# Optimization experiments

Measured on AMD Instinct MI355X. Metric: run time of the kernel, lower is better.

The kernel has to match this reference:

```python
import jax, jax.numpy as jnp
import numpy as np

N, E, G = 50000, 800000, 128
IN_DIM, HID, HEADS, OUT_DIM = 256, 64, 4, 10
HC = HID * HEADS  # 256
NEG_SLOPE = 0.2


def _gat_layer(x, src, dst, W, att_src, att_dst, bias):
    # x: [N, F_in]; W: [F_in, H*C]; att_*: [H, C]; bias: [H*C]
    n = x.shape[0]
    h = (x @ W).reshape(n, HEADS, HID)                      # [N,H,C]
    a_src = jnp.einsum('nhc,hc->nh', h, att_src)            # [N,H]
    a_dst = jnp.einsum('nhc,hc->nh', h, att_dst)            # [N,H]
    e = a_src[src] + a_dst[dst]                             # [E,H]
    e = jax.nn.leaky_relu(e, NEG_SLOPE)
    # segment softmax over incoming edges of each dst node
    m = jax.ops.segment_max(e, dst, num_segments=n)         # [N,H]
    ex = jnp.exp(e - m[dst])
    denom = jax.ops.segment_sum(ex, dst, num_segments=n)    # [N,H]
    alpha = ex / (denom[dst] + 1e-16)                       # [E,H]
    msg = h[src] * alpha[:, :, None]                        # [E,H,C]
    out = jax.ops.segment_sum(msg, dst, num_segments=n)     # [N,H,C]
    return out.reshape(n, HC) + bias


def setup_inputs() -> dict:
    key = jax.random.key(0)
    ks = jax.random.split(key, 16)
    x = jax.random.normal(ks[0], (N, IN_DIM), dtype=jnp.float32)
    edge_index = jax.random.randint(ks[1], (2, E), 0, N, dtype=jnp.int64)
    edge_weight = jax.random.uniform(ks[2], (E,), dtype=jnp.float32)
    batch = jnp.sort(jax.random.randint(ks[3], (N,), 0, G, dtype=jnp.int64))
    s = 0.05
    W1 = jax.random.normal(ks[4], (IN_DIM, HC), dtype=jnp.float32) * s
    att_src1 = jax.random.normal(ks[5], (HEADS, HID), dtype=jnp.float32) * s
    att_dst1 = jax.random.normal(ks[6], (HEADS, HID), dtype=jnp.float32) * s
    b1 = jnp.zeros((HC,), dtype=jnp.float32)
    W2 = jax.random.normal(ks[7], (HC, HC), dtype=jnp.float32) * s
    att_src2 = jax.random.normal(ks[8], (HEADS, HID), dtype=jnp.float32) * s
    att_dst2 = jax.random.normal(ks[9], (HEADS, HID), dtype=jnp.float32) * s
    b2 = jnp.zeros((HC,), dtype=jnp.float32)
    Wf = jax.random.normal(ks[10], (HC, OUT_DIM), dtype=jnp.float32) * s
    bf = jnp.zeros((OUT_DIM,), dtype=jnp.float32)
    return dict(x=x, edge_index=edge_index, edge_weight=edge_weight, batch=batch,
                W1=W1, att_src1=att_src1, att_dst1=att_dst1, b1=b1,
                W2=W2, att_src2=att_src2, att_dst2=att_dst2, b2=b2,
                Wf=Wf, bf=bf)


def reference(x, edge_index, edge_weight, batch,
              W1, att_src1, att_dst1, b1,
              W2, att_src2, att_dst2, b2,
              Wf, bf):
    n = x.shape[0]
    # add self loops (add_self_loops=True in GATConv)
    loop = jnp.arange(n, dtype=edge_index.dtype)
    ei = jnp.concatenate([edge_index, jnp.stack([loop, loop])], axis=1)
    src, dst = ei[0], ei[1]
    h = jax.nn.relu(_gat_layer(x, src, dst, W1, att_src1, att_dst1, b1))
    h = jax.nn.relu(_gat_layer(h, src, dst, W2, att_src2, att_dst2, b2))
    # global mean pool per graph
    counts = jax.ops.segment_sum(jnp.ones((n,), dtype=h.dtype), batch, num_segments=G)
    pooled = jax.ops.segment_sum(h, batch, num_segments=G) / jnp.maximum(counts, 1.0)[:, None]
    out = pooled @ Wf + bf
    return out, pooled
```

## Files before the change

### kernel.cpp

```cpp
#include <hip/hip_runtime.h>
#include <math.h>

#define HEADS 4
#define HID 64
#define HC 256
#define NEG_SLOPE 0.2f
#define GG 128

typedef __attribute__((ext_vector_type(8))) short short8;
typedef __attribute__((ext_vector_type(4))) float floatx4;

__device__ __forceinline__ unsigned short f2bf(float f) {
  unsigned u = __float_as_uint(f);
  unsigned r = (u + 0x7FFFu + ((u >> 16) & 1u)) >> 16;
  return (unsigned short)r;
}
__device__ __forceinline__ float bf2f(unsigned short h) {
  return __uint_as_float(((unsigned)h) << 16);
}

__global__ void fill_counts_kernel(int* counts, int n) {
  int i = blockIdx.x * 256 + threadIdx.x;
  if (i < n) counts[i] = 1;
}

__global__ void hist_kernel(const int* __restrict__ ei, int* counts, int E) {
  int e = blockIdx.x * 256 + threadIdx.x;
  if (e < E) atomicAdd(&counts[ei[E + e]], 1);
}

__global__ __launch_bounds__(256) void scan_pass1(const int* __restrict__ counts,
                                                  int* __restrict__ bsums, int n) {
  int t = threadIdx.x;
  int i0 = blockIdx.x * 1024 + t * 4;
  int s = 0;
  if (i0 + 3 < n) {
    int4 v = *(const int4*)&counts[i0];
    s = v.x + v.y + v.z + v.w;
  } else {
#pragma unroll
    for (int k = 0; k < 4; ++k)
      if (i0 + k < n) s += counts[i0 + k];
  }
#pragma unroll
  for (int o = 1; o < 64; o <<= 1) s += __shfl_xor(s, o, 64);
  __shared__ int ws[4];
  if ((t & 63) == 0) ws[t >> 6] = s;
  __syncthreads();
  if (t == 0) bsums[blockIdx.x] = ws[0] + ws[1] + ws[2] + ws[3];
}

__global__ __launch_bounds__(256) void scan_pass2(int* __restrict__ bsums,
                                                  int* __restrict__ row_ptr, int nb, int n) {
  __shared__ int sh[256];
  int t = threadIdx.x;
  int v = (t < nb) ? bsums[t] : 0;
  sh[t] = v;
  __syncthreads();
  for (int off = 1; off < 256; off <<= 1) {
    int u = (t >= off) ? sh[t - off] : 0;
    __syncthreads();
    sh[t] += u;
    __syncthreads();
  }
  if (t < nb) bsums[t] = sh[t] - v;
  if (t == 255) row_ptr[n] = sh[255];
}

__global__ __launch_bounds__(256) void scan_pass3(const int* __restrict__ counts,
                                                  const int* __restrict__ bsums,
                                                  int* __restrict__ row_ptr,
                                                  int* __restrict__ cursor, int n) {
  int t = threadIdx.x;
  int i0 = blockIdx.x * 1024 + t * 4;
  int c0 = 0, c1 = 0, c2 = 0, c3 = 0;
  bool full = (i0 + 3 < n);
  if (full) {
    int4 v = *(const int4*)&counts[i0];
    c0 = v.x; c1 = v.y; c2 = v.z; c3 = v.w;
  } else {
    if (i0 + 0 < n) c0 = counts[i0 + 0];
    if (i0 + 1 < n) c1 = counts[i0 + 1];
    if (i0 + 2 < n) c2 = counts[i0 + 2];
    if (i0 + 3 < n) c3 = counts[i0 + 3];
  }
  int ts = c0 + c1 + c2 + c3;
  __shared__ int sh[256];
  sh[t] = ts;
  __syncthreads();
  for (int off = 1; off < 256; off <<= 1) {
    int u = (t >= off) ? sh[t - off] : 0;
    __syncthreads();
    sh[t] += u;
    __syncthreads();
  }
  int run = bsums[blockIdx.x] + sh[t] - ts;
  int r0 = run, r1 = run + c0, r2 = r1 + c1, r3 = r2 + c2;
  if (full) {
    *(int4*)&row_ptr[i0] = make_int4(r0, r1, r2, r3);
    *(int4*)&cursor[i0] = make_int4(r0, r1, r2, r3);
  } else {
    if (i0 + 0 < n) { row_ptr[i0 + 0] = r0; cursor[i0 + 0] = r0; }
    if (i0 + 1 < n) { row_ptr[i0 + 1] = r1; cursor[i0 + 1] = r1; }
    if (i0 + 2 < n) { row_ptr[i0 + 2] = r2; cursor[i0 + 2] = r2; }
    if (i0 + 3 < n) { row_ptr[i0 + 3] = r3; cursor[i0 + 3] = r3; }
  }
}

__global__ void scatter_kernel(const int* __restrict__ ei, int* cursor, int* srcs, int E, int n) {
  int i = blockIdx.x * 256 + threadIdx.x;
  if (i >= E + n) return;
  int s, d;
  if (i < E) { s = ei[i]; d = ei[E + i]; }
  else       { s = i - E; d = s; }
  int pos = atomicAdd(&cursor[d], 1);
  srcs[pos] = s;
}

__global__ void convertB_kernel(const float* __restrict__ B, unsigned short* __restrict__ Bth,
                                unsigned short* __restrict__ Btl) {
  int k = blockIdx.x, n = threadIdx.x;
  float v = B[k * HC + n];
  unsigned short h = f2bf(v);
  unsigned short l = f2bf(v - bf2f(h));
  Bth[n * HC + k] = h;
  Btl[n * HC + k] = l;
}

#define LDA 40
__global__ __launch_bounds__(256) void gemm_kernel(
    const float* __restrict__ A, const unsigned short* __restrict__ Bth,
    const unsigned short* __restrict__ Btl, const float* __restrict__ att_src,
    const float* __restrict__ att_dst, unsigned short* __restrict__ Cb,
    float* __restrict__ asrc_o, float* __restrict__ adst_o, int M) {
  __shared__ unsigned short sAh[128 * LDA];
  __shared__ unsigned short sAl[128 * LDA];
  __shared__ unsigned short sBh[128 * LDA];
  __shared__ unsigned short sBl[128 * LDA];

  int t = threadIdx.x;
  int lane = t & 63, wave = t >> 6;
  int wm = wave >> 1, wn = wave & 1;
  int q = lane >> 4, mrow = lane & 15;
  int r0 = blockIdx.y * 128;
  int c0 = blockIdx.x * 128;

  int arow = t >> 1;
  int aofs = (t & 1) * 16;
  bool avalid = (r0 + arow) < M;
  const float* Ag = A + (size_t)(r0 + arow) * HC + aofs;
  const unsigned short* Bgh = Bth + (size_t)(c0 + arow) * HC + aofs;
  const unsigned short* Bgl = Btl + (size_t)(c0 + arow) * HC + aofs;

  floatx4 acc[4][4];
#pragma unroll
  for (int i = 0; i < 4; ++i)
#pragma unroll
    for (int j = 0; j < 4; ++j) acc[i][j] = (floatx4)(0.0f);

  for (int k0 = 0; k0 < HC; k0 += 32) {
    __syncthreads();
#pragma unroll
    for (int c = 0; c < 16; c += 4) {
      float4 v = make_float4(0.f, 0.f, 0.f, 0.f);
      if (avalid) v = *(const float4*)(Ag + k0 + c);
      unsigned short h0 = f2bf(v.x), h1 = f2bf(v.y), h2 = f2bf(v.z), h3 = f2bf(v.w);
      ushort4 hv = make_ushort4(h0, h1, h2, h3);
      ushort4 lv = make_ushort4(f2bf(v.x - bf2f(h0)), f2bf(v.y - bf2f(h1)),
                                f2bf(v.z - bf2f(h2)), f2bf(v.w - bf2f(h3)));
      *(ushort4*)&sAh[arow * LDA + aofs + c] = hv;
      *(ushort4*)&sAl[arow * LDA + aofs + c] = lv;
    }
    *(int4*)&sBh[arow * LDA + aofs] = *(const int4*)(Bgh + k0);
    *(int4*)&sBh[arow * LDA + aofs + 8] = *(const int4*)(Bgh + k0 + 8);
    *(int4*)&sBl[arow * LDA + aofs] = *(const int4*)(Bgl + k0);
    *(int4*)&sBl[arow * LDA + aofs + 8] = *(const int4*)(Bgl + k0 + 8);
    __syncthreads();

    short8 ah[4], al[4], bh[4], bl[4];
#pragma unroll
    for (int i = 0; i < 4; ++i) {
      int ar = (wm * 64 + i * 16 + mrow) * LDA + q * 8;
      int br = (wn * 64 + i * 16 + mrow) * LDA + q * 8;
      ah[i] = *(short8*)&sAh[ar];
      al[i] = *(short8*)&sAl[ar];
      bh[i] = *(short8*)&sBh[br];
      bl[i] = *(short8*)&sBl[br];
    }
#pragma unroll
    for (int i = 0; i < 4; ++i)
#pragma unroll
      for (int j = 0; j < 4; ++j) {
        acc[i][j] = __builtin_amdgcn_mfma_f32_16x16x32_bf16(ah[i], bh[j], acc[i][j], 0, 0, 0);
        acc[i][j] = __builtin_amdgcn_mfma_f32_16x16x32_bf16(ah[i], bl[j], acc[i][j], 0, 0, 0);
        acc[i][j] = __builtin_amdgcn_mfma_f32_16x16x32_bf16(al[i], bh[j], acc[i][j], 0, 0, 0);
      }
  }

  int hd = (c0 >> 6) + wn;
  float aS[4], aD[4];
#pragma unroll
  for (int j = 0; j < 4; ++j) {
    aS[j] = att_src[hd * 64 + j * 16 + mrow];
    aD[j] = att_dst[hd * 64 + j * 16 + mrow];
  }
#pragma unroll
  for (int i = 0; i < 4; ++i) {
#pragma unroll
    for (int r = 0; r < 4; ++r) {
      float ps = acc[i][0][r] * aS[0] + acc[i][1][r] * aS[1] +
                 acc[i][2][r] * aS[2] + acc[i][3][r] * aS[3];
      float pd = acc[i][0][r] * aD[0] + acc[i][1][r] * aD[1] +
                 acc[i][2][r] * aD[2] + acc[i][3][r] * aD[3];
#pragma unroll
      for (int o = 1; o < 16; o <<= 1) {
        ps += __shfl_xor(ps, o, 64);
        pd += __shfl_xor(pd, o, 64);
      }
      int grow = r0 + wm * 64 + i * 16 + q * 4 + r;
      if (mrow == 0 && grow < M) {
        asrc_o[grow * HEADS + hd] = ps;
        adst_o[grow * HEADS + hd] = pd;
      }
    }
  }

#pragma unroll
  for (int i = 0; i < 4; ++i) {
#pragma unroll
    for (int j = 0; j < 4; ++j) {
      int col = c0 + wn * 64 + j * 16 + mrow;
#pragma unroll
      for (int r = 0; r < 4; ++r) {
        int grow = r0 + wm * 64 + i * 16 + q * 4 + r;
        if (grow < M) Cb[(size_t)grow * HC + col] = f2bf(acc[i][j][r]);
      }
    }
  }
}

__device__ __forceinline__ float lrelu(float x) { return x > 0.f ? x : NEG_SLOPE * x; }

__global__ __launch_bounds__(256) void aggregate_kernel(
    const unsigned short* __restrict__ hbf, const float* __restrict__ asrc,
    const float* __restrict__ adst, const int* __restrict__ row_ptr,
    const int* __restrict__ srcs, const float* __restrict__ bias,
    float* __restrict__ hout, int N) {
  __shared__ float s_alpha[4][64 * 4];
  __shared__ int s_src[4][64];

  int wave = threadIdx.x >> 6;
  int lane = threadIdx.x & 63;
  int node = blockIdx.x * 4 + wave;
  if (node >= N) return;

  int begin = row_ptr[node];
  int end = row_ptr[node + 1];
  int deg = end - begin;
  int nb = deg < 64 ? deg : 64;

  const float4* asrc4 = (const float4*)asrc;
  float4 ad = ((const float4*)adst)[node];

  const float NEGINF = -3.402823466e38f;
  int s0 = 0;
  float4 e0 = make_float4(NEGINF, NEGINF, NEGINF, NEGINF);
  if (lane < nb) {
    s0 = srcs[begin + lane];
    float4 a = asrc4[s0];
    e0.x = lrelu(a.x + ad.x);
    e0.y = lrelu(a.y + ad.y);
    e0.z = lrelu(a.z + ad.z);
    e0.w = lrelu(a.w + ad.w);
  }
  float m0 = e0.x, m1 = e0.y, m2 = e0.z, m3 = e0.w;
  for (int base = 64; base < deg; base += 64) {
    int idx = base + lane;
    if (idx < deg) {
      int s = srcs[begin + idx];
      float4 a = asrc4[s];
      m0 = fmaxf(m0, lrelu(a.x + ad.x));
      m1 = fmaxf(m1, lrelu(a.y + ad.y));
      m2 = fmaxf(m2, lrelu(a.z + ad.z));
      m3 = fmaxf(m3, lrelu(a.w + ad.w));
    }
  }
#pragma unroll
  for (int o = 1; o < 64; o <<= 1) {
    m0 = fmaxf(m0, __shfl_xor(m0, o, 64));
    m1 = fmaxf(m1, __shfl_xor(m1, o, 64));
    m2 = fmaxf(m2, __shfl_xor(m2, o, 64));
    m3 = fmaxf(m3, __shfl_xor(m3, o, 64));
  }
  float ex0 = (lane < nb) ? __expf(e0.x - m0) : 0.f;
  float ex1 = (lane < nb) ? __expf(e0.y - m1) : 0.f;
  float ex2 = (lane < nb) ? __expf(e0.z - m2) : 0.f;
  float ex3 = (lane < nb) ? __expf(e0.w - m3) : 0.f;
  float d0 = ex0, d1 = ex1, d2 = ex2, d3 = ex3;
  for (int base = 64; base < deg; base += 64) {
    int idx = base + lane;
    if (idx < deg) {
      int s = srcs[begin + idx];
      float4 a = asrc4[s];
      d0 += __expf(lrelu(a.x + ad.x) - m0);
      d1 += __expf(lrelu(a.y + ad.y) - m1);
      d2 += __expf(lrelu(a.z + ad.z) - m2);
      d3 += __expf(lrelu(a.w + ad.w) - m3);
    }
  }
#pragma unroll
  for (int o = 1; o < 64; o <<= 1) {
    d0 += __shfl_xor(d0, o, 64);
    d1 += __shfl_xor(d1, o, 64);
    d2 += __shfl_xor(d2, o, 64);
    d3 += __shfl_xor(d3, o, 64);
  }
  float r0 = 1.0f / (d0 + 1e-16f);
  float r1 = 1.0f / (d1 + 1e-16f);
  float r2 = 1.0f / (d2 + 1e-16f);
  float r3 = 1.0f / (d3 + 1e-16f);

  *(float4*)&s_alpha[wave][lane * 4] = make_float4(ex0 * r0, ex1 * r1, ex2 * r2, ex3 * r3);
  s_src[wave][lane] = s0;

  int head = lane >> 4;
  float mh = (head == 0) ? m0 : (head == 1) ? m1 : (head == 2) ? m2 : m3;
  float rdh = (head == 0) ? r0 : (head == 1) ? r1 : (head == 2) ? r2 : r3;
  float adh = (head == 0) ? ad.x : (head == 1) ? ad.y : (head == 2) ? ad.z : ad.w;

  const ushort4* hb4 = (const ushort4*)hbf;
  float4 accA = make_float4(0.f, 0.f, 0.f, 0.f);
  float4 accB = accA, accC = accA, accD = accA;
  int i = 0;
  for (; i + 4 <= nb; i += 4) {
    int sa = s_src[wave][i];
    int sb = s_src[wave][i + 1];
    int sc = s_src[wave][i + 2];
    int sd = s_src[wave][i + 3];
    float aa = s_alpha[wave][i * 4 + head];
    float ab = s_alpha[wave][(i + 1) * 4 + head];
    float ac = s_alpha[wave][(i + 2) * 4 + head];
    float ad_ = s_alpha[wave][(i + 3) * 4 + head];
    ushort4 u0 = hb4[(size_t)sa * 64 + lane];
    ushort4 u1 = hb4[(size_t)sb * 64 + lane];
    ushort4 u2 = hb4[(size_t)sc * 64 + lane];
    ushort4 u3 = hb4[(size_t)sd * 64 + lane];
    accA.x += aa * bf2f(u0.x); accA.y += aa * bf2f(u0.y);
    accA.z += aa * bf2f(u0.z); accA.w += aa * bf2f(u0.w);
    accB.x += ab * bf2f(u1.x); accB.y += ab * bf2f(u1.y);
    accB.z += ab * bf2f(u1.z); accB.w += ab * bf2f(u1.w);
    accC.x += ac * bf2f(u2.x); accC.y += ac * bf2f(u2.y);
    accC.z += ac * bf2f(u2.z); accC.w += ac * bf2f(u2.w);
    accD.x += ad_ * bf2f(u3.x); accD.y += ad_ * bf2f(u3.y);
    accD.z += ad_ * bf2f(u3.z); accD.w += ad_ * bf2f(u3.w);
  }
  for (; i < nb; ++i) {
    int s = s_src[wave][i];
    float a = s_alpha[wave][i * 4 + head];
    ushort4 u = hb4[(size_t)s * 64 + lane];
    accA.x += a * bf2f(u.x); accA.y += a * bf2f(u.y);
    accA.z += a * bf2f(u.z); accA.w += a * bf2f(u.w);
  }
  for (int i2 = 64; i2 < deg; ++i2) {
    int s = srcs[begin + i2];
    float ash = asrc[s * HEADS + head];
    float a = __expf(lrelu(ash + adh) - mh) * rdh;
    ushort4 u = hb4[(size_t)s * 64 + lane];
    accA.x += a * bf2f(u.x); accA.y += a * bf2f(u.y);
    accA.z += a * bf2f(u.z); accA.w += a * bf2f(u.w);
  }

  float4 acc;
  acc.x = (accA.x + accB.x) + (accC.x + accD.x);
  acc.y = (accA.y + accB.y) + (accC.y + accD.y);
  acc.z = (accA.z + accB.z) + (accC.z + accD.z);
  acc.w = (accA.w + accB.w) + (accC.w + accD.w);
  float4 bv = ((const float4*)bias)[lane];
  float4 o;
  o.x = fmaxf(acc.x + bv.x, 0.f);
  o.y = fmaxf(acc.y + bv.y, 0.f);
  o.z = fmaxf(acc.z + bv.z, 0.f);
  o.w = fmaxf(acc.w + bv.w, 0.f);
  ((float4*)hout)[(size_t)node * 64 + lane] = o;
}

__device__ __forceinline__ int lower_bound_i(const int* a, int n, int key) {
  int lo = 0, hi = n;
  while (lo < hi) {
    int mid = (lo + hi) >> 1;
    if (a[mid] < key) lo = mid + 1; else hi = mid;
  }
  return lo;
}

__global__ __launch_bounds__(256) void pool_kernel(const float* __restrict__ h2,
                                                   const int* __restrict__ batch,
                                                   float* __restrict__ pooled, int n) {
  int g = blockIdx.x;
  int wave = threadIdx.x >> 6, lane = threadIdx.x & 63;
  int lo = lower_bound_i(batch, n, g);
  int hi = lower_bound_i(batch, n, g + 1);
  const float4* h4 = (const float4*)h2;
  float4 acc = make_float4(0.f, 0.f, 0.f, 0.f);
  for (int i = lo + wave; i < hi; i += 4) {
    float4 v = h4[(size_t)i * 64 + lane];
    acc.x += v.x; acc.y += v.y; acc.z += v.z; acc.w += v.w;
  }
  __shared__ float4 red[4][64];
  red[wave][lane] = acc;
  __syncthreads();
  if (wave == 0) {
    float4 a0 = red[0][lane], a1 = red[1][lane], a2 = red[2][lane], a3 = red[3][lane];
    float inv = 1.0f / fmaxf((float)(hi - lo), 1.0f);
    float4 o;
    o.x = (a0.x + a1.x + a2.x + a3.x) * inv;
    o.y = (a0.y + a1.y + a2.y + a3.y) * inv;
    o.z = (a0.z + a1.z + a2.z + a3.z) * inv;
    o.w = (a0.w + a1.w + a2.w + a3.w) * inv;
    ((float4*)pooled)[g * 64 + lane] = o;
  }
}

__global__ void final_kernel(const float* __restrict__ pooled, const float* __restrict__ Wf,
                             const float* __restrict__ bf, float* __restrict__ out) {
  int g = blockIdx.x, t = threadIdx.x;
  __shared__ float p[HC];
  p[t] = pooled[g * HC + t];
  __syncthreads();
  if (t < 10) {
    float s = bf[t];
    for (int c = 0; c < HC; ++c) s += p[c] * Wf[c * 10 + t];
    out[g * 10 + t] = s;
  }
}

extern "C" void kernel_launch(void* const* d_in, const int* in_sizes, int n_in,
                              void* d_out, int out_size, void* d_ws, size_t ws_size,
                              hipStream_t stream) {
  const float* x    = (const float*)d_in[0];
  const int*   ei   = (const int*)d_in[1];
  const int*   batch = (const int*)d_in[3];
  const float* W1   = (const float*)d_in[4];
  const float* as1  = (const float*)d_in[5];
  const float* ad1  = (const float*)d_in[6];
  const float* b1   = (const float*)d_in[7];
  const float* W2   = (const float*)d_in[8];
  const float* as2  = (const float*)d_in[9];
  const float* ad2  = (const float*)d_in[10];
  const float* b2   = (const float*)d_in[11];
  const float* Wf   = (const float*)d_in[12];
  const float* bf   = (const float*)d_in[13];
  float* out = (float*)d_out;

  const int N = in_sizes[0] / HC;
  const int E = in_sizes[1] / 2;

  float* bufB = (float*)d_ws;
  unsigned short* hbf = (unsigned short*)(bufB + (size_t)N * HC);
  float* asrc = (float*)(hbf + (size_t)N * HC);
  float* adst = asrc + (size_t)N * HEADS;
  int* counts = (int*)(adst + (size_t)N * HEADS);
  int* row_ptr = counts + N;
  int* cursor = row_ptr + N + 1;
  int* srcs = cursor + N;
  int* bsums = srcs + E + N;
  unsigned short* Bth = (unsigned short*)(bsums + ((N + 1023) / 1024 + 4));
  unsigned short* Btl = Bth + HC * HC;

  int nb = (N + 1023) / 1024;

  fill_counts_kernel<<<(N + 255) / 256, 256, 0, stream>>>(counts, N);
  hist_kernel<<<(E + 255) / 256, 256, 0, stream>>>(ei, counts, E);
  scan_pass1<<<nb, 256, 0, stream>>>(counts, bsums, N);
  scan_pass2<<<1, 256, 0, stream>>>(bsums, row_ptr, nb, N);
  scan_pass3<<<nb, 256, 0, stream>>>(counts, bsums, row_ptr, cursor, N);
  scatter_kernel<<<(E + N + 255) / 256, 256, 0, stream>>>(ei, cursor, srcs, E, N);

  dim3 ggrid(2, (N + 127) / 128);
  int agg_blocks = (N + 3) / 4;

  convertB_kernel<<<HC, HC, 0, stream>>>(W1, Bth, Btl);
  gemm_kernel<<<ggrid, 256, 0, stream>>>(x, Bth, Btl, as1, ad1, hbf, asrc, adst, N);
  aggregate_kernel<<<agg_blocks, 256, 0, stream>>>(hbf, asrc, adst, row_ptr, srcs, b1, bufB, N);

  convertB_kernel<<<HC, HC, 0, stream>>>(W2, Bth, Btl);
  gemm_kernel<<<ggrid, 256, 0, stream>>>(bufB, Bth, Btl, as2, ad2, hbf, asrc, adst, N);
  aggregate_kernel<<<agg_blocks, 256, 0, stream>>>(hbf, asrc, adst, row_ptr, srcs, b2, bufB, N);

  pool_kernel<<<GG, 256, 0, stream>>>(bufB, batch, out + GG * 10, N);
  final_kernel<<<GG, 256, 0, stream>>>(out + GG * 10, Wf, bf, out);
}
```

Measured before the change: 495.4 us.

## Pre-split GEMM A operand into bf16 hi/lo and parallelize pooling

Adds a splitA kernel that converts x into bf16 high/low halves once, and has layer-1 aggregation write its output directly as bf16 hi/lo. The GEMM then loads pre-split bf16 tiles with int4 loads instead of converting fp32 inside the inner loop. Pooling is split across 4 partial blocks per graph, and the final kernel reduces the partials. The intent is to remove redundant per-tile conversion (A was re-split for each of the 2 column blocks) and raise pooling parallelism. The cost is an extra pass over x and a reworked workspace layout.

```diff
diff --git a/kernel.cpp b/kernel.cpp
--- a/kernel.cpp
+++ b/kernel.cpp
@@ -9,13 +9,14 @@
 
 typedef __attribute__((ext_vector_type(8))) short short8;
 typedef __attribute__((ext_vector_type(4))) float floatx4;
-
-__device__ __forceinline__ unsigned short f2bf(float f) {
+typedef unsigned short ush;
+
+__device__ __forceinline__ ush f2bf(float f) {
   unsigned u = __float_as_uint(f);
   unsigned r = (u + 0x7FFFu + ((u >> 16) & 1u)) >> 16;
-  return (unsigned short)r;
-}
-__device__ __forceinline__ float bf2f(unsigned short h) {
+  return (ush)r;
+}
+__device__ __forceinline__ float bf2f(ush h) {
   return __uint_as_float(((unsigned)h) << 16);
 }
 
@@ -117,26 +118,47 @@
   srcs[pos] = s;
 }
 
-__global__ void convertB_kernel(const float* __restrict__ B, unsigned short* __restrict__ Bth,
-                                unsigned short* __restrict__ Btl) {
+__global__ __launch_bounds__(256) void splitA_kernel(const float* __restrict__ A,
+                                                     ush* __restrict__ Ah,
+                                                     ush* __restrict__ Al, int total) {
+  int i0 = (blockIdx.x * 256 + threadIdx.x) * 4;
+  if (i0 + 3 < total) {
+    float4 v = *(const float4*)&A[i0];
+    ushort4 h = make_ushort4(f2bf(v.x), f2bf(v.y), f2bf(v.z), f2bf(v.w));
+    ushort4 l = make_ushort4(f2bf(v.x - bf2f(h.x)), f2bf(v.y - bf2f(h.y)),
+                             f2bf(v.z - bf2f(h.z)), f2bf(v.w - bf2f(h.w)));
+    *(ushort4*)&Ah[i0] = h;
+    *(ushort4*)&Al[i0] = l;
+  } else {
+    for (int k = 0; k < 4 && i0 + k < total; ++k) {
+      float v = A[i0 + k];
+      ush h = f2bf(v);
+      Ah[i0 + k] = h;
+      Al[i0 + k] = f2bf(v - bf2f(h));
+    }
+  }
+}
+
+__global__ void convertB_kernel(const float* __restrict__ B, ush* __restrict__ Bth,
+                                ush* __restrict__ Btl) {
   int k = blockIdx.x, n = threadIdx.x;
   float v = B[k * HC + n];
-  unsigned short h = f2bf(v);
-  unsigned short l = f2bf(v - bf2f(h));
+  ush h = f2bf(v);
+  ush l = f2bf(v - bf2f(h));
   Bth[n * HC + k] = h;
   Btl[n * HC + k] = l;
 }
 
 #define LDA 40
 __global__ __launch_bounds__(256) void gemm_kernel(
-    const float* __restrict__ A, const unsigned short* __restrict__ Bth,
-    const unsigned short* __restrict__ Btl, const float* __restrict__ att_src,
-    const float* __restrict__ att_dst, unsigned short* __restrict__ Cb,
-    float* __restrict__ asrc_o, float* __restrict__ adst_o, int M) {
-  __shared__ unsigned short sAh[128 * LDA];
-  __shared__ unsigned short sAl[128 * LDA];
-  __shared__ unsigned short sBh[128 * LDA];
-  __shared__ unsigned short sBl[128 * LDA];
+    const ush* __restrict__ Ah, const ush* __restrict__ Al,
+    const ush* __restrict__ Bth, const ush* __restrict__ Btl,
+    const float* __restrict__ att_src, const float* __restrict__ att_dst,
+    ush* __restrict__ Cb, float* __restrict__ asrc_o, float* __restrict__ adst_o, int M) {
+  __shared__ ush sAh[128 * LDA];
+  __shared__ ush sAl[128 * LDA];
+  __shared__ ush sBh[128 * LDA];
+  __shared__ ush sBl[128 * LDA];
 
   int t = threadIdx.x;
   int lane = t & 63, wave = t >> 6;
@@ -145,12 +167,10 @@
   int r0 = blockIdx.y * 128;
   int c0 = blockIdx.x * 128;
 
-  int arow = t >> 1;
-  int aofs = (t & 1) * 16;
-  bool avalid = (r0 + arow) < M;
-  const float* Ag = A + (size_t)(r0 + arow) * HC + aofs;
-  const unsigned short* Bgh = Bth + (size_t)(c0 + arow) * HC + aofs;
-  const unsigned short* Bgl = Btl + (size_t)(c0 + arow) * HC + aofs;
+  int row0 = t >> 2, seg0 = t & 3;
+  int row1 = (t + 256) >> 2, seg1 = (t + 256) & 3;
+  bool v0 = (r0 + row0) < M, v1 = (r0 + row1) < M;
+  const int4 zero4 = make_int4(0, 0, 0, 0);
 
   floatx4 acc[4][4];
 #pragma unroll
@@ -160,21 +180,20 @@
 
   for (int k0 = 0; k0 < HC; k0 += 32) {
     __syncthreads();
-#pragma unroll
-    for (int c = 0; c < 16; c += 4) {
-      float4 v = make_float4(0.f, 0.f, 0.f, 0.f);
-      if (avalid) v = *(const float4*)(Ag + k0 + c);
-      unsigned short h0 = f2bf(v.x), h1 = f2bf(v.y), h2 = f2bf(v.z), h3 = f2bf(v.w);
-      ushort4 hv = make_ushort4(h0, h1, h2, h3);
-      ushort4 lv = make_ushort4(f2bf(v.x - bf2f(h0)), f2bf(v.y - bf2f(h1)),
-                                f2bf(v.z - bf2f(h2)), f2bf(v.w - bf2f(h3)));
-      *(ushort4*)&sAh[arow * LDA + aofs + c] = hv;
-      *(ushort4*)&sAl[arow * LDA + aofs + c] = lv;
-    }
-    *(int4*)&sBh[arow * LDA + aofs] = *(const int4*)(Bgh + k0);
-    *(int4*)&sBh[arow * LDA + aofs + 8] = *(const int4*)(Bgh + k0 + 8);
-    *(int4*)&sBl[arow * LDA + aofs] = *(const int4*)(Bgl + k0);
-    *(int4*)&sBl[arow * LDA + aofs + 8] = *(const int4*)(Bgl + k0 + 8);
+    {
+      size_t g0 = (size_t)(r0 + row0) * HC + k0 + seg0 * 8;
+      size_t g1 = (size_t)(r0 + row1) * HC + k0 + seg1 * 8;
+      *(int4*)&sAh[row0 * LDA + seg0 * 8] = v0 ? *(const int4*)&Ah[g0] : zero4;
+      *(int4*)&sAh[row1 * LDA + seg1 * 8] = v1 ? *(const int4*)&Ah[g1] : zero4;
+      *(int4*)&sAl[row0 * LDA + seg0 * 8] = v0 ? *(const int4*)&Al[g0] : zero4;
+      *(int4*)&sAl[row1 * LDA + seg1 * 8] = v1 ? *(const int4*)&Al[g1] : zero4;
+      size_t b0 = (size_t)(c0 + row0) * HC + k0 + seg0 * 8;
+      size_t b1 = (size_t)(c0 + row1) * HC + k0 + seg1 * 8;
+      *(int4*)&sBh[row0 * LDA + seg0 * 8] = *(const int4*)&Bth[b0];
+      *(int4*)&sBh[row1 * LDA + seg1 * 8] = *(const int4*)&Bth[b1];
+      *(int4*)&sBl[row0 * LDA + seg0 * 8] = *(const int4*)&Btl[b0];
+      *(int4*)&sBl[row1 * LDA + seg1 * 8] = *(const int4*)&Btl[b1];
+    }
     __syncthreads();
 
     short8 ah[4], al[4], bh[4], bl[4];
@@ -242,10 +261,10 @@
 __device__ __forceinline__ float lrelu(float x) { return x > 0.f ? x : NEG_SLOPE * x; }
 
 __global__ __launch_bounds__(256) void aggregate_kernel(
-    const unsigned short* __restrict__ hbf, const float* __restrict__ asrc,
+    const ush* __restrict__ hbf, const float* __restrict__ asrc,
     const float* __restrict__ adst, const int* __restrict__ row_ptr,
     const int* __restrict__ srcs, const float* __restrict__ bias,
-    float* __restrict__ hout, int N) {
+    float* __restrict__ outf, ush* __restrict__ outh, ush* __restrict__ outl, int N) {
   __shared__ float s_alpha[4][64 * 4];
   __shared__ int s_src[4][64];
 
@@ -381,7 +400,16 @@
   o.y = fmaxf(acc.y + bv.y, 0.f);
   o.z = fmaxf(acc.z + bv.z, 0.f);
   o.w = fmaxf(acc.w + bv.w, 0.f);
-  ((float4*)hout)[(size_t)node * 64 + lane] = o;
+
+  if (outf) {
+    ((float4*)outf)[(size_t)node * 64 + lane] = o;
+  } else {
+    ushort4 h = make_ushort4(f2bf(o.x), f2bf(o.y), f2bf(o.z), f2bf(o.w));
+    ushort4 l = make_ushort4(f2bf(o.x - bf2f(h.x)), f2bf(o.y - bf2f(h.y)),
+                             f2bf(o.z - bf2f(h.z)), f2bf(o.w - bf2f(h.w)));
+    ((ushort4*)outh)[(size_t)node * 64 + lane] = h;
+    ((ushort4*)outl)[(size_t)node * 64 + lane] = l;
+  }
 }
 
 __device__ __forceinline__ int lower_bound_i(const int* a, int n, int key) {
@@ -395,14 +423,15 @@
 
 __global__ __launch_bounds__(256) void pool_kernel(const float* __restrict__ h2,
                                                    const int* __restrict__ batch,
-                                                   float* __restrict__ pooled, int n) {
-  int g = blockIdx.x;
+                                                   float* __restrict__ pws,
+                                                   int* __restrict__ cnts, int n) {
+  int g = blockIdx.x, part = blockIdx.y;
   int wave = threadIdx.x >> 6, lane = threadIdx.x & 63;
   int lo = lower_bound_i(batch, n, g);
   int hi = lower_bound_i(batch, n, g + 1);
   const float4* h4 = (const float4*)h2;
   float4 acc = make_float4(0.f, 0.f, 0.f, 0.f);
-  for (int i = lo + wave; i < hi; i += 4) {
+  for (int i = lo + part * 4 + wave; i < hi; i += 16) {
     float4 v = h4[(size_t)i * 64 + lane];
     acc.x += v.x; acc.y += v.y; acc.z += v.z; acc.w += v.w;
   }
@@ -411,26 +440,32 @@
   __syncthreads();
   if (wave == 0) {
     float4 a0 = red[0][lane], a1 = red[1][lane], a2 = red[2][lane], a3 = red[3][lane];
-    float inv = 1.0f / fmaxf((float)(hi - lo), 1.0f);
     float4 o;
-    o.x = (a0.x + a1.x + a2.x + a3.x) * inv;
-    o.y = (a0.y + a1.y + a2.y + a3.y) * inv;
-    o.z = (a0.z + a1.z + a2.z + a3.z) * inv;
-    o.w = (a0.w + a1.w + a2.w + a3.w) * inv;
-    ((float4*)pooled)[g * 64 + lane] = o;
-  }
-}
-
-__global__ void final_kernel(const float* __restrict__ pooled, const float* __restrict__ Wf,
-                             const float* __restrict__ bf, float* __restrict__ out) {
+    o.x = (a0.x + a1.x) + (a2.x + a3.x);
+    o.y = (a0.y + a1.y) + (a2.y + a3.y);
+    o.z = (a0.z + a1.z) + (a2.z + a3.z);
+    o.w = (a0.w + a1.w) + (a2.w + a3.w);
+    ((float4*)pws)[(size_t)(g * 4 + part) * 64 + lane] = o;
+  }
+  if (part == 0 && threadIdx.x == 0) cnts[g] = hi - lo;
+}
+
+__global__ void final_kernel(const float* __restrict__ pws, const int* __restrict__ cnts,
+                             const float* __restrict__ Wf, const float* __restrict__ bf,
+                             float* __restrict__ pooled_out, float* __restrict__ out) {
   int g = blockIdx.x, t = threadIdx.x;
+  float s = pws[(size_t)(g * 4 + 0) * 256 + t] + pws[(size_t)(g * 4 + 1) * 256 + t] +
+            pws[(size_t)(g * 4 + 2) * 256 + t] + pws[(size_t)(g * 4 + 3) * 256 + t];
+  float inv = 1.0f / fmaxf((float)cnts[g], 1.0f);
+  float pv = s * inv;
+  pooled_out[g * HC + t] = pv;
   __shared__ float p[HC];
-  p[t] = pooled[g * HC + t];
+  p[t] = pv;
   __syncthreads();
   if (t < 10) {
-    float s = bf[t];
-    for (int c = 0; c < HC; ++c) s += p[c] * Wf[c * 10 + t];
-    out[g * 10 + t] = s;
+    float acc = bf[t];
+    for (int c = 0; c < HC; ++c) acc += p[c] * Wf[c * 10 + t];
+    out[g * 10 + t] = acc;
   }
 }
 
@@ -455,17 +490,28 @@
   const int N = in_sizes[0] / HC;
   const int E = in_sizes[1] / 2;
 
-  float* bufB = (float*)d_ws;
-  unsigned short* hbf = (unsigned short*)(bufB + (size_t)N * HC);
-  float* asrc = (float*)(hbf + (size_t)N * HC);
-  float* adst = asrc + (size_t)N * HEADS;
-  int* counts = (int*)(adst + (size_t)N * HEADS);
-  int* row_ptr = counts + N;
-  int* cursor = row_ptr + N + 1;
-  int* srcs = cursor + N;
-  int* bsums = srcs + E + N;
-  unsigned short* Bth = (unsigned short*)(bsums + ((N + 1023) / 1024 + 4));
-  unsigned short* Btl = Bth + HC * HC;
+  char* base = (char*)d_ws;
+  size_t off = 0;
+  auto alloc = [&](size_t bytes) {
+    char* p = base + off;
+    off = (off + bytes + 255) & ~(size_t)255;
+    return p;
+  };
+  ush* xh = (ush*)alloc((size_t)N * HC * 2);
+  ush* xl = (ush*)alloc((size_t)N * HC * 2);
+  float* bufB = (float*)xh;
+  ush* hbf = (ush*)alloc((size_t)N * HC * 2);
+  float* asrc = (float*)alloc((size_t)N * HEADS * 4);
+  float* adst = (float*)alloc((size_t)N * HEADS * 4);
+  int* counts = (int*)alloc((size_t)N * 4);
+  int* row_ptr = (int*)alloc((size_t)(N + 1) * 4);
+  int* cursor = (int*)alloc((size_t)N * 4);
+  int* srcs = (int*)alloc((size_t)(E + N) * 4);
+  int* bsums = (int*)alloc(((N + 1023) / 1024) * 4);
+  ush* Bth = (ush*)alloc((size_t)HC * HC * 2);
+  ush* Btl = (ush*)alloc((size_t)HC * HC * 2);
+  float* pws = (float*)alloc((size_t)GG * 4 * HC * 4);
+  int* cnts = (int*)alloc((size_t)GG * 4);
 
   int nb = (N + 1023) / 1024;
 
@@ -479,14 +525,19 @@
   dim3 ggrid(2, (N + 127) / 128);
   int agg_blocks = (N + 3) / 4;
 
+  splitA_kernel<<<(N * HC / 4 + 255) / 256, 256, 0, stream>>>(x, xh, xl, N * HC);
+
   convertB_kernel<<<HC, HC, 0, stream>>>(W1, Bth, Btl);
-  gemm_kernel<<<ggrid, 256, 0, stream>>>(x, Bth, Btl, as1, ad1, hbf, asrc, adst, N);
-  aggregate_kernel<<<agg_blocks, 256, 0, stream>>>(hbf, asrc, adst, row_ptr, srcs, b1, bufB, N);
+  gemm_kernel<<<ggrid, 256, 0, stream>>>(xh, xl, Bth, Btl, as1, ad1, hbf, asrc, adst, N);
+  aggregate_kernel<<<agg_blocks, 256, 0, stream>>>(hbf, asrc, adst, row_ptr, srcs, b1,
+                                                   nullptr, xh, xl, N);
 
   convertB_kernel<<<HC, HC, 0, stream>>>(W2, Bth, Btl);
-  gemm_kernel<<<ggrid, 256, 0, stream>>>(bufB, Bth, Btl, as2, ad2, hbf, asrc, adst, N);
-  aggregate_kernel<<<agg_blocks, 256, 0, stream>>>(hbf, asrc, adst, row_ptr, srcs, b2, bufB, N);
-
-  pool_kernel<<<GG, 256, 0, stream>>>(bufB, batch, out + GG * 10, N);
-  final_kernel<<<GG, 256, 0, stream>>>(out + GG * 10, Wf, bf, out);
-}
+  gemm_kernel<<<ggrid, 256, 0, stream>>>(xh, xl, Bth, Btl, as2, ad2, hbf, asrc, adst, N);
+  aggregate_kernel<<<agg_blocks, 256, 0, stream>>>(hbf, asrc, adst, row_ptr, srcs, b2,
+                                                   bufB, nullptr, nullptr, N);
+
+  dim3 pgrid(GG, 4);
+  pool_kernel<<<pgrid, 256, 0, stream>>>(bufB, batch, pws, cnts, N);
+  final_kernel<<<GG, 256, 0, stream>>>(pws, cnts, Wf, bf, out + GG * 10, out);
+}
```

Measured after the change: 482.3 us. -2.6%, faster.
